# Kernel tuning notes

Hardware: AMD Instinct MI355X
Metric: run time of the kernel (lower is better)

Reference implementation:

```python
import jax, jax.numpy as jnp
import numpy as np

EPS = 1e-5

def _ln(x, g, b):
    m = jnp.mean(x, axis=-1, keepdims=True)
    v = jnp.mean((x - m) ** 2, axis=-1, keepdims=True)
    return (x - m) * jax.lax.rsqrt(v + EPS) * g + b


def setup_inputs() -> dict:
    key = jax.random.key(0)
    B, T, C, H, A = 4, 1024, 1024, 16, 64
    ks = jax.random.split(key, 16)
    s = 0.02
    inp = {
        "x": jax.random.normal(ks[0], (B, T, C), jnp.float32),
        "ln1_g": jnp.ones((C,), jnp.float32), "ln1_b": jnp.zeros((C,), jnp.float32),
        "ln2_g": jnp.ones((C,), jnp.float32), "ln2_b": jnp.zeros((C,), jnp.float32),
        "ln3_g": jnp.ones((C,), jnp.float32), "ln3_b": jnp.zeros((C,), jnp.float32),
        "wq": jax.random.normal(ks[1], (C, C), jnp.float32) * s, "bq": jnp.zeros((C,), jnp.float32),
        "wk": jax.random.normal(ks[2], (C, C), jnp.float32) * s, "bk": jnp.zeros((C,), jnp.float32),
        "wv": jax.random.normal(ks[3], (C, C), jnp.float32) * s, "bv": jnp.zeros((C,), jnp.float32),
        "wo": jax.random.normal(ks[4], (C, C), jnp.float32) * s, "bo": jnp.zeros((C,), jnp.float32),
        "w1": jax.random.normal(ks[5], (C, 4 * C), jnp.float32) * s, "b1": jnp.zeros((4 * C,), jnp.float32),
        "w2": jax.random.normal(ks[6], (4 * C, C), jnp.float32) * s, "b2": jnp.zeros((C,), jnp.float32),
        "wd": jax.random.normal(ks[7], (C, A), jnp.float32) * 1e-4, "bd": jnp.zeros((A,), jnp.float32),
        "wu": jax.random.normal(ks[8], (A, C), jnp.float32) * 1e-4, "bu": jnp.zeros((C,), jnp.float32),
    }
    return inp


def _block(x, ln1_g, ln1_b, ln2_g, ln2_b, ln3_g, ln3_b,
           wq, bq, wk, bk, wv, bv, wo, bo, w1, b1, w2, b2, wd, bd, wu, bu):
    B, T, C = x.shape
    H = 16
    D = C // H
    normed = _ln(x, ln3_g, ln3_b)  # ln3 of original input, used by adapter

    # --- causal self-attention on ln1(x) ---
    h = _ln(x, ln1_g, ln1_b)
    q = (h @ wq + bq).reshape(B, T, H, D)
    k = (h @ wk + bk).reshape(B, T, H, D)
    v = (h @ wv + bv).reshape(B, T, H, D)
    att = jnp.einsum('bqhd,bkhd->bhqk', q, k) * (1.0 / np.sqrt(D))
    causal = jnp.tril(jnp.ones((T, T), bool))
    att = jnp.where(causal, att, -jnp.inf)
    att = jax.nn.softmax(att, axis=-1)
    y = jnp.einsum('bhqk,bkhd->bqhd', att, v).reshape(B, T, C)
    attn_out = y @ wo + bo

    hidden = x + attn_out
    # --- MLP on ln2(hidden) ---
    m = _ln(hidden, ln2_g, ln2_b)
    mlp_out = jax.nn.gelu(m @ w1 + b1, approximate=False) @ w2 + b2
    forward_states = hidden + mlp_out

    # --- adapter on ln3(original x) ---
    a = jax.nn.relu(normed @ wd + bd) @ wu + bu

    # dropout is identity (p=0 / eval)
    return hidden + forward_states + a


def reference(x, ln1_g, ln1_b, ln2_g, ln2_b, ln3_g, ln3_b,
              wq, bq, wk, bk, wv, bv, wo, bo, w1, b1, w2, b2, wd, bd, wu, bu):
    return _block(x, ln1_g, ln1_b, ln2_g, ln2_b, ln3_g, ln3_b,
                  wq, bq, wk, bk, wv, bv, wo, bo, w1, b1, w2, b2, wd, bd, wu, bu)
```

## Files before the change

### kernel.cpp

```cpp
#include <hip/hip_runtime.h>

typedef unsigned short u16;
typedef __bf16 bf16x8 __attribute__((ext_vector_type(8)));
typedef u16    u16x8  __attribute__((ext_vector_type(8)));
typedef float  f32x4  __attribute__((ext_vector_type(4)));

__device__ __forceinline__ u16 f2bf(float f) {
    union { float f; unsigned u; } x{f};
    unsigned r = x.u + 0x7fffu + ((x.u >> 16) & 1u);
    return (u16)(r >> 16);
}

__device__ __forceinline__ f32x4 mfma16(bf16x8 a, bf16x8 b, f32x4 c) {
    return __builtin_amdgcn_mfma_f32_16x16x32_bf16(a, b, c, 0, 0, 0);
}

__global__ void transpose_to_bf16(const float* __restrict__ in, u16* __restrict__ out,
                                  int K, int N) {
    __shared__ float tile[32][33];
    const int k0 = blockIdx.y * 32, n0 = blockIdx.x * 32;
    for (int i = threadIdx.y; i < 32; i += 8)
        tile[i][threadIdx.x] = in[(long)(k0 + i) * N + n0 + threadIdx.x];
    __syncthreads();
    for (int i = threadIdx.y; i < 32; i += 8)
        out[(long)(n0 + i) * K + k0 + threadIdx.x] = f2bf(tile[threadIdx.x][i]);
}

__global__ void concat_bias(const float* __restrict__ bq, const float* __restrict__ bk,
                            const float* __restrict__ bv, float* __restrict__ out) {
    int i = blockIdx.x * 256 + threadIdx.x;
    out[i] = i < 1024 ? bq[i] : (i < 2048 ? bk[i - 1024] : bv[i - 2048]);
}

__global__ void ln_dual_kernel(const float* __restrict__ x,
                               const float* __restrict__ g1, const float* __restrict__ b1,
                               const float* __restrict__ g3, const float* __restrict__ b3,
                               u16* __restrict__ out1, u16* __restrict__ out3) {
    const int row = blockIdx.x;
    const long base = (long)row * 1024;
    const int t = threadIdx.x;
    float4 v = ((const float4*)(x + base))[t];
    float s = v.x + v.y + v.z + v.w;
    float ss = v.x * v.x + v.y * v.y + v.z * v.z + v.w * v.w;
    for (int o = 32; o > 0; o >>= 1) { s += __shfl_down(s, o); ss += __shfl_down(ss, o); }
    __shared__ float red[8];
    if ((t & 63) == 0) { red[t >> 6] = s; red[(t >> 6) + 4] = ss; }
    __syncthreads();
    float sum = red[0] + red[1] + red[2] + red[3];
    float sq  = red[4] + red[5] + red[6] + red[7];
    const float mean = sum * (1.f / 1024.f);
    const float rstd = rsqrtf(sq * (1.f / 1024.f) - mean * mean + 1e-5f);
    float4 G1 = ((const float4*)g1)[t], B1 = ((const float4*)b1)[t];
    float4 G3 = ((const float4*)g3)[t], B3 = ((const float4*)b3)[t];
    float n0 = (v.x - mean) * rstd, n1 = (v.y - mean) * rstd;
    float n2 = (v.z - mean) * rstd, n3 = (v.w - mean) * rstd;
    ushort4 o1, o3;
    o1.x = f2bf(n0 * G1.x + B1.x); o1.y = f2bf(n1 * G1.y + B1.y);
    o1.z = f2bf(n2 * G1.z + B1.z); o1.w = f2bf(n3 * G1.w + B1.w);
    o3.x = f2bf(n0 * G3.x + B3.x); o3.y = f2bf(n1 * G3.y + B3.y);
    o3.z = f2bf(n2 * G3.z + B3.z); o3.w = f2bf(n3 * G3.w + B3.w);
    ((ushort4*)(out1 + base))[t] = o1;
    ((ushort4*)(out3 + base))[t] = o3;
}

__global__ void ln_single_kernel(const float* __restrict__ x,
                                 const float* __restrict__ g, const float* __restrict__ b,
                                 u16* __restrict__ out) {
    const int row = blockIdx.x;
    const long base = (long)row * 1024;
    const int t = threadIdx.x;
    float4 v = ((const float4*)(x + base))[t];
    float s = v.x + v.y + v.z + v.w;
    float ss = v.x * v.x + v.y * v.y + v.z * v.z + v.w * v.w;
    for (int o = 32; o > 0; o >>= 1) { s += __shfl_down(s, o); ss += __shfl_down(ss, o); }
    __shared__ float red[8];
    if ((t & 63) == 0) { red[t >> 6] = s; red[(t >> 6) + 4] = ss; }
    __syncthreads();
    float sum = red[0] + red[1] + red[2] + red[3];
    float sq  = red[4] + red[5] + red[6] + red[7];
    const float mean = sum * (1.f / 1024.f);
    const float rstd = rsqrtf(sq * (1.f / 1024.f) - mean * mean + 1e-5f);
    float4 G = ((const float4*)g)[t], B = ((const float4*)b)[t];
    ushort4 o;
    o.x = f2bf((v.x - mean) * rstd * G.x + B.x);
    o.y = f2bf((v.y - mean) * rstd * G.y + B.y);
    o.z = f2bf((v.z - mean) * rstd * G.z + B.z);
    o.w = f2bf((v.w - mean) * rstd * G.w + B.w);
    ((ushort4*)(out + base))[t] = o;
}

__global__ void transpose_v(const u16* __restrict__ qkv, u16* __restrict__ vT) {
    const int bh = blockIdx.z, b = bh >> 4, hh = bh & 15;
    const int t0 = blockIdx.x * 32, d0 = blockIdx.y * 32;
    __shared__ u16 tile[32][33];
    const u16* src = qkv + (long)(b * 1024) * 3072 + 2048 + hh * 64;
    for (int i = threadIdx.y; i < 32; i += 8)
        tile[i][threadIdx.x] = src[(long)(t0 + i) * 3072 + d0 + threadIdx.x];
    __syncthreads();
    u16* dst = vT + (long)bh * 64 * 1024;
    for (int i = threadIdx.y; i < 32; i += 8)
        dst[(long)(d0 + i) * 1024 + t0 + threadIdx.x] = tile[threadIdx.x][i];
}

template <typename Epi>
__global__ __launch_bounds__(256, 2)
void gemm_kernel(const u16* __restrict__ A, const u16* __restrict__ Bt,
                 int M, int N, int K, Epi epi) {
    __shared__ u16 smA[128 * 32];
    __shared__ u16 smB[128 * 32];
    const int tid = threadIdx.x;
    const int m0 = blockIdx.y * 128;
    const int n0 = blockIdx.x * 128;
    const int wid = tid >> 6, lane = tid & 63;
    const int wm = (wid >> 1) * 64, wn = (wid & 1) * 64;
    const int lr = lane & 15, lh = lane >> 4;

    const int c0 = tid, c1 = tid + 256;
    const int ar0 = c0 >> 2, as0 = (c0 & 3) * 8;
    const int ar1 = c1 >> 2, as1 = (c1 & 3) * 8;
    const long aoff0 = (long)(m0 + ar0) * K + as0;
    const long aoff1 = (long)(m0 + ar1) * K + as1;
    const long boff0 = (long)min(n0 + ar0, N - 1) * K + as0;
    const long boff1 = (long)min(n0 + ar1, N - 1) * K + as1;

    f32x4 acc[4][4] = {};

    uint4 ra0 = *(const uint4*)(A + aoff0);
    uint4 ra1 = *(const uint4*)(A + aoff1);
    uint4 rb0 = *(const uint4*)(Bt + boff0);
    uint4 rb1 = *(const uint4*)(Bt + boff1);

    const int nk = K / 32;
    for (int kt = 0; kt < nk; ++kt) {
        __syncthreads();
        *(uint4*)(smA + c0 * 8) = ra0;
        *(uint4*)(smA + c1 * 8) = ra1;
        *(uint4*)(smB + c0 * 8) = rb0;
        *(uint4*)(smB + c1 * 8) = rb1;
        __syncthreads();
        if (kt + 1 < nk) {
            const int ko = (kt + 1) * 32;
            ra0 = *(const uint4*)(A + aoff0 + ko);
            ra1 = *(const uint4*)(A + aoff1 + ko);
            rb0 = *(const uint4*)(Bt + boff0 + ko);
            rb1 = *(const uint4*)(Bt + boff1 + ko);
        }
        bf16x8 af[4], bfr[4];
#pragma unroll
        for (int i = 0; i < 4; ++i)
            af[i] = *(const bf16x8*)(smA + (wm + i * 16 + lr) * 32 + lh * 8);
#pragma unroll
        for (int j = 0; j < 4; ++j)
            bfr[j] = *(const bf16x8*)(smB + (wn + j * 16 + lr) * 32 + lh * 8);
#pragma unroll
        for (int i = 0; i < 4; ++i)
#pragma unroll
            for (int j = 0; j < 4; ++j)
                acc[i][j] = mfma16(af[i], bfr[j], acc[i][j]);
    }

#pragma unroll
    for (int i = 0; i < 4; ++i)
#pragma unroll
        for (int j = 0; j < 4; ++j) {
            const int col = n0 + wn + j * 16 + lr;
            if (col < N) {
#pragma unroll
                for (int r = 0; r < 4; ++r) {
                    const int row = m0 + wm + i * 16 + lh * 4 + r;
                    epi(row, col, acc[i][j][r]);
                }
            }
        }
}

struct EpiBF16Bias {
    u16* out; const float* bias; int ldo;
    __device__ void operator()(int r, int c, float v) const {
        out[(long)r * ldo + c] = f2bf(v + bias[c]);
    }
};
struct EpiResid {
    float* hidden; const float* bias; const float* x;
    __device__ void operator()(int r, int c, float v) const {
        long i = (long)r * 1024 + c; hidden[i] = v + bias[c] + x[i];
    }
};
struct EpiGelu {
    u16* out; const float* bias;
    __device__ void operator()(int r, int c, float v) const {
        float x = v + bias[c];
        float g = 0.5f * x * (1.f + erff(x * 0.70710678118654752f));
        out[(long)r * 4096 + c] = f2bf(g);
    }
};
struct EpiReluBF16 {
    u16* out; const float* bias;
    __device__ void operator()(int r, int c, float v) const {
        out[(long)r * 64 + c] = f2bf(fmaxf(v + bias[c], 0.f));
    }
};
struct EpiAdapter {
    float* out; const float* bias; const float* hidden;
    __device__ void operator()(int r, int c, float v) const {
        long i = (long)r * 1024 + c; out[i] = 2.f * hidden[i] + v + bias[c];
    }
};
struct EpiAddOut {
    float* out; const float* bias;
    __device__ void operator()(int r, int c, float v) const {
        long i = (long)r * 1024 + c; out[i] += v + bias[c];
    }
};

__global__ __launch_bounds__(256, 2)
void attn_kernel(const u16* __restrict__ qkv, const u16* __restrict__ vT,
                 u16* __restrict__ y) {
    const int bh = blockIdx.x, b = bh >> 4, hh = bh & 15;
    const int q0 = blockIdx.y * 128;
    const int tid = threadIdx.x, wid = tid >> 6, lane = tid & 63;
    const int lr = lane & 15, lh = lane >> 4;
    const int qw = q0 + wid * 32;

    __shared__ u16 smK[64 * 72];
    __shared__ u16 smV[64 * 72];
    __shared__ u16 smP[4 * 32 * 72];
    u16* pw = smP + wid * (32 * 72);

    const u16* qbase = qkv + (long)(b * 1024) * 3072 + hh * 64;
    const u16* kbase = qbase + 1024;
    const u16* vbase = vT + (long)bh * 64 * 1024;

    bf16x8 a_q[2][2];
#pragma unroll
    for (int mt = 0; mt < 2; ++mt)
#pragma unroll
        for (int ks = 0; ks < 2; ++ks) {
            uint4 t = *(const uint4*)(qbase + (long)(qw + mt * 16 + lr) * 3072 + ks * 32 + lh * 8);
            a_q[mt][ks] = __builtin_bit_cast(bf16x8, t);
        }

    bf16x8 ones;
    { u16x8 t = {0x3F80, 0x3F80, 0x3F80, 0x3F80, 0x3F80, 0x3F80, 0x3F80, 0x3F80};
      ones = __builtin_bit_cast(bf16x8, t); }

    f32x4 o_acc[2][4] = {};
    f32x4 l_acc[2] = {};
    f32x4 m_run[2] = {{-1e30f, -1e30f, -1e30f, -1e30f}, {-1e30f, -1e30f, -1e30f, -1e30f}};

    const int ntiles = q0 / 64 + 2;
    const int ck = tid >> 3, cs = (tid & 7) * 8;
    const int ck2 = (tid + 256) >> 3, cs2 = ((tid + 256) & 7) * 8;
    for (int kt = 0; kt < ntiles; ++kt) {
        const int k0 = kt * 64;
        __syncthreads();
        {
            uint4 kv0 = *(const uint4*)(kbase + (long)(k0 + ck) * 3072 + cs);
            uint4 kv1 = *(const uint4*)(kbase + (long)(k0 + ck2) * 3072 + cs2);
            *(uint4*)(smK + ck * 72 + cs) = kv0;
            *(uint4*)(smK + ck2 * 72 + cs2) = kv1;
            uint4 vv0 = *(const uint4*)(vbase + (long)ck * 1024 + k0 + cs);
            uint4 vv1 = *(const uint4*)(vbase + (long)ck2 * 1024 + k0 + cs2);
            *(uint4*)(smV + ck * 72 + cs) = vv0;
            *(uint4*)(smV + ck2 * 72 + cs2) = vv1;
        }
        __syncthreads();
        if (k0 > qw + 31) continue;

        bf16x8 bK[4][2];
#pragma unroll
        for (int nt = 0; nt < 4; ++nt)
#pragma unroll
            for (int ks = 0; ks < 2; ++ks)
                bK[nt][ks] = *(const bf16x8*)(smK + (nt * 16 + lr) * 72 + ks * 32 + lh * 8);

        f32x4 s[2][4];
#pragma unroll
        for (int mt = 0; mt < 2; ++mt)
#pragma unroll
            for (int nt = 0; nt < 4; ++nt) {
                f32x4 z = {0.f, 0.f, 0.f, 0.f};
                z = mfma16(a_q[mt][0], bK[nt][0], z);
                z = mfma16(a_q[mt][1], bK[nt][1], z);
                s[mt][nt] = z;
            }
#pragma unroll
        for (int mt = 0; mt < 2; ++mt) {
            const int qb = qw + mt * 16 + lh * 4;
#pragma unroll
            for (int nt = 0; nt < 4; ++nt) {
                const int kkg = k0 + nt * 16 + lr;
#pragma unroll
                for (int r = 0; r < 4; ++r) {
                    float v = s[mt][nt][r] * 0.125f;
                    if (kkg > qb + r) v = -1e30f;
                    s[mt][nt][r] = v;
                }
            }
        }
#pragma unroll
        for (int mt = 0; mt < 2; ++mt) {
            f32x4 mx = s[mt][0];
#pragma unroll
            for (int nt = 1; nt < 4; ++nt)
#pragma unroll
                for (int r = 0; r < 4; ++r) mx[r] = fmaxf(mx[r], s[mt][nt][r]);
#pragma unroll
            for (int xm = 1; xm < 16; xm <<= 1)
#pragma unroll
                for (int r = 0; r < 4; ++r) mx[r] = fmaxf(mx[r], __shfl_xor(mx[r], xm));
            f32x4 mnew, alpha;
#pragma unroll
            for (int r = 0; r < 4; ++r) {
                mnew[r] = fmaxf(m_run[mt][r], mx[r]);
                alpha[r] = __expf(m_run[mt][r] - mnew[r]);
            }
            m_run[mt] = mnew;
            l_acc[mt] *= alpha;
#pragma unroll
            for (int dt = 0; dt < 4; ++dt) o_acc[mt][dt] *= alpha;
#pragma unroll
            for (int nt = 0; nt < 4; ++nt)
#pragma unroll
                for (int r = 0; r < 4; ++r)
                    s[mt][nt][r] = __expf(s[mt][nt][r] - mnew[r]);
#pragma unroll
            for (int nt = 0; nt < 4; ++nt)
#pragma unroll
                for (int r = 0; r < 4; ++r)
                    pw[(mt * 16 + lh * 4 + r) * 72 + nt * 16 + lr] = f2bf(s[mt][nt][r]);
        }
        bf16x8 vf[4][2];
#pragma unroll
        for (int dt = 0; dt < 4; ++dt)
#pragma unroll
            for (int ks = 0; ks < 2; ++ks)
                vf[dt][ks] = *(const bf16x8*)(smV + (dt * 16 + lr) * 72 + ks * 32 + lh * 8);
#pragma unroll
        for (int mt = 0; mt < 2; ++mt) {
            bf16x8 pf0 = *(const bf16x8*)(pw + (mt * 16 + lr) * 72 + lh * 8);
            bf16x8 pf1 = *(const bf16x8*)(pw + (mt * 16 + lr) * 72 + 32 + lh * 8);
            l_acc[mt] = mfma16(pf0, ones, l_acc[mt]);
            l_acc[mt] = mfma16(pf1, ones, l_acc[mt]);
#pragma unroll
            for (int dt = 0; dt < 4; ++dt) {
                o_acc[mt][dt] = mfma16(pf0, vf[dt][0], o_acc[mt][dt]);
                o_acc[mt][dt] = mfma16(pf1, vf[dt][1], o_acc[mt][dt]);
            }
        }
    }
#pragma unroll
    for (int mt = 0; mt < 2; ++mt) {
        f32x4 linv;
#pragma unroll
        for (int r = 0; r < 4; ++r) linv[r] = 1.f / l_acc[mt][r];
#pragma unroll
        for (int dt = 0; dt < 4; ++dt) {
#pragma unroll
            for (int r = 0; r < 4; ++r) {
                const int tok = b * 1024 + qw + mt * 16 + lh * 4 + r;
                y[(long)tok * 1024 + hh * 64 + dt * 16 + lr] = f2bf(o_acc[mt][dt][r] * linv[r]);
            }
        }
    }
}

extern "C" void kernel_launch(void* const* d_in, const int* in_sizes, int n_in,
                              void* d_out, int out_size, void* d_ws, size_t ws_size,
                              hipStream_t stream) {
    const float* x    = (const float*)d_in[0];
    const float* ln1g = (const float*)d_in[1];
    const float* ln1b = (const float*)d_in[2];
    const float* ln2g = (const float*)d_in[3];
    const float* ln2b = (const float*)d_in[4];
    const float* ln3g = (const float*)d_in[5];
    const float* ln3b = (const float*)d_in[6];
    const float* wq = (const float*)d_in[7];  const float* bq = (const float*)d_in[8];
    const float* wk = (const float*)d_in[9];  const float* bk = (const float*)d_in[10];
    const float* wv = (const float*)d_in[11]; const float* bv = (const float*)d_in[12];
    const float* wo = (const float*)d_in[13]; const float* bo = (const float*)d_in[14];
    const float* w1 = (const float*)d_in[15]; const float* b1 = (const float*)d_in[16];
    const float* w2 = (const float*)d_in[17]; const float* b2 = (const float*)d_in[18];
    const float* wd = (const float*)d_in[19]; const float* bd = (const float*)d_in[20];
    const float* wu = (const float*)d_in[21]; const float* bu = (const float*)d_in[22];
    float* out = (float*)d_out;

    char* base = (char*)d_ws;
    size_t off = 0;
    auto carve = [&](size_t bytes) -> char* {
        char* p = base + off; off += (bytes + 255) & ~(size_t)255; return p;
    };
    u16* qkv_wt = (u16*)carve(3072L * 1024 * 2);
    u16* wo_t   = (u16*)carve(1024L * 1024 * 2);
    u16* w1_t   = (u16*)carve(4096L * 1024 * 2);
    u16* w2_t   = (u16*)carve(1024L * 4096 * 2);
    u16* wd_t   = (u16*)carve(64L * 1024 * 2);
    u16* wu_t   = (u16*)carve(1024L * 64 * 2);
    float* bqkv = (float*)carve(3072L * 4);
    u16* hbuf   = (u16*)carve(4096L * 1024 * 2);
    u16* nrm    = (u16*)carve(4096L * 1024 * 2);
    u16* qkvb   = (u16*)carve(4096L * 3072 * 2);
    u16* vT     = (u16*)carve(64L * 64 * 1024 * 2);
    u16* ybuf   = (u16*)carve(4096L * 1024 * 2);
    float* hid  = (float*)carve(4096L * 1024 * 4);
    u16* mbuf   = (u16*)carve(4096L * 1024 * 2);
    u16* act    = (u16*)carve(4096L * 4096 * 2);
    u16* t1     = (u16*)carve(4096L * 64 * 2);

    const dim3 tb(32, 8);
    transpose_to_bf16<<<dim3(32, 32), tb, 0, stream>>>(wq, qkv_wt, 1024, 1024);
    transpose_to_bf16<<<dim3(32, 32), tb, 0, stream>>>(wk, qkv_wt + 1024L * 1024, 1024, 1024);
    transpose_to_bf16<<<dim3(32, 32), tb, 0, stream>>>(wv, qkv_wt + 2048L * 1024, 1024, 1024);
    transpose_to_bf16<<<dim3(32, 32), tb, 0, stream>>>(wo, wo_t, 1024, 1024);
    transpose_to_bf16<<<dim3(128, 32), tb, 0, stream>>>(w1, w1_t, 1024, 4096);
    transpose_to_bf16<<<dim3(32, 128), tb, 0, stream>>>(w2, w2_t, 4096, 1024);
    transpose_to_bf16<<<dim3(2, 32), tb, 0, stream>>>(wd, wd_t, 1024, 64);
    transpose_to_bf16<<<dim3(32, 2), tb, 0, stream>>>(wu, wu_t, 64, 1024);
    concat_bias<<<12, 256, 0, stream>>>(bq, bk, bv, bqkv);

    ln_dual_kernel<<<4096, 256, 0, stream>>>(x, ln1g, ln1b, ln3g, ln3b, hbuf, nrm);

    gemm_kernel<<<dim3(24, 32), 256, 0, stream>>>(hbuf, qkv_wt, 4096, 3072, 1024,
                                                  EpiBF16Bias{qkvb, bqkv, 3072});
    transpose_v<<<dim3(32, 2, 64), tb, 0, stream>>>(qkvb, vT);
    attn_kernel<<<dim3(64, 8), 256, 0, stream>>>(qkvb, vT, ybuf);
    gemm_kernel<<<dim3(8, 32), 256, 0, stream>>>(ybuf, wo_t, 4096, 1024, 1024,
                                                 EpiResid{hid, bo, x});
    ln_single_kernel<<<4096, 256, 0, stream>>>(hid, ln2g, ln2b, mbuf);
    gemm_kernel<<<dim3(32, 32), 256, 0, stream>>>(mbuf, w1_t, 4096, 4096, 1024,
                                                  EpiGelu{act, b1});
    gemm_kernel<<<dim3(1, 32), 256, 0, stream>>>(nrm, wd_t, 4096, 64, 1024,
                                                 EpiReluBF16{t1, bd});
    gemm_kernel<<<dim3(8, 32), 256, 0, stream>>>(t1, wu_t, 4096, 1024, 64,
                                                 EpiAdapter{out, bu, hid});
    gemm_kernel<<<dim3(8, 32), 256, 0, stream>>>(act, w2_t, 4096, 1024, 4096,
                                                 EpiAddOut{out, b2});
}
```

Measured before the change: 471.0 us.

## Load GEMM tiles directly into LDS with swizzle and widen weight transpose

The GEMM main loop now uses global_load_lds to copy A/B tiles straight from global memory into LDS, replacing the register-staged prefetch. An XOR swizzle on the 16-byte chunks is applied to the LDS layout to avoid bank conflicts on the fragment reads. Launch bounds are raised to 3 blocks per CU. The weight transpose/convert kernel moves to 64x64 tiles with float4 loads and ushort4 stores. The register prefetch that overlapped the next tile's global load with the MFMAs is gone, so load latency is exposed each iteration unless the extra occupancy hides it.

After: 488.4 us. 3.7% more time.

```diff
diff --git a/kernel.cpp b/kernel.cpp
--- a/kernel.cpp
+++ b/kernel.cpp
@@ -15,15 +15,36 @@
     return __builtin_amdgcn_mfma_f32_16x16x32_bf16(a, b, c, 0, 0, 0);
 }
 
+__device__ __forceinline__ void async_ld16(const void* g, void* l) {
+    __builtin_amdgcn_global_load_lds(
+        (const __attribute__((address_space(1))) unsigned int*)g,
+        (__attribute__((address_space(3))) unsigned int*)l, 16, 0, 0);
+}
+
 __global__ void transpose_to_bf16(const float* __restrict__ in, u16* __restrict__ out,
                                   int K, int N) {
-    __shared__ float tile[32][33];
-    const int k0 = blockIdx.y * 32, n0 = blockIdx.x * 32;
-    for (int i = threadIdx.y; i < 32; i += 8)
-        tile[i][threadIdx.x] = in[(long)(k0 + i) * N + n0 + threadIdx.x];
+    __shared__ float tile[64][65];
+    const int k0 = blockIdx.y * 64, n0 = blockIdx.x * 64;
+    const int tid = threadIdx.x;
+    const int rr = tid >> 4, cc = tid & 15;
+#pragma unroll
+    for (int it = 0; it < 4; ++it) {
+        const int r = rr + it * 16;
+        float4 v = *(const float4*)(in + (long)(k0 + r) * N + n0 + cc * 4);
+        tile[r][cc * 4 + 0] = v.x; tile[r][cc * 4 + 1] = v.y;
+        tile[r][cc * 4 + 2] = v.z; tile[r][cc * 4 + 3] = v.w;
+    }
     __syncthreads();
-    for (int i = threadIdx.y; i < 32; i += 8)
-        out[(long)(n0 + i) * K + k0 + threadIdx.x] = f2bf(tile[threadIdx.x][i]);
+#pragma unroll
+    for (int it = 0; it < 4; ++it) {
+        const int n = rr + it * 16;
+        ushort4 o;
+        o.x = f2bf(tile[cc * 4 + 0][n]);
+        o.y = f2bf(tile[cc * 4 + 1][n]);
+        o.z = f2bf(tile[cc * 4 + 2][n]);
+        o.w = f2bf(tile[cc * 4 + 3][n]);
+        *(ushort4*)(out + (long)(n0 + n) * K + k0 + cc * 4) = o;
+    }
 }
 
 __global__ void concat_bias(const float* __restrict__ bq, const float* __restrict__ bk,
@@ -103,7 +124,7 @@
 }
 
 template <typename Epi>
-__global__ __launch_bounds__(256, 2)
+__global__ __launch_bounds__(256, 3)
 void gemm_kernel(const u16* __restrict__ A, const u16* __restrict__ Bt,
                  int M, int N, int K, Epi epi) {
     __shared__ u16 smA[128 * 32];
@@ -115,43 +136,45 @@
     const int wm = (wid >> 1) * 64, wn = (wid & 1) * 64;
     const int lr = lane & 15, lh = lane >> 4;
 
-    const int c0 = tid, c1 = tid + 256;
-    const int ar0 = c0 >> 2, as0 = (c0 & 3) * 8;
-    const int ar1 = c1 >> 2, as1 = (c1 & 3) * 8;
-    const long aoff0 = (long)(m0 + ar0) * K + as0;
-    const long aoff1 = (long)(m0 + ar1) * K + as1;
-    const long boff0 = (long)min(n0 + ar0, N - 1) * K + as0;
-    const long boff1 = (long)min(n0 + ar1, N - 1) * K + as1;
+    const int cr = lane >> 2;
+    const int lq = lane & 3;
+    const int r0 = wid * 32 + cr;
+    const int r1 = wid * 32 + 16 + cr;
+    const int q0 = lq ^ (r0 & 3) ^ ((r0 >> 2) & 3);
+    const int q1 = lq ^ (r1 & 3) ^ ((r1 >> 2) & 3);
+    const int br0 = min(n0 + r0, N - 1);
+    const int br1 = min(n0 + r1, N - 1);
+    const long aoff0 = (long)(m0 + r0) * K + q0 * 8;
+    const long aoff1 = (long)(m0 + r1) * K + q1 * 8;
+    const long boff0 = (long)br0 * K + q0 * 8;
+    const long boff1 = (long)br1 * K + q1 * 8;
+    u16* ldsA0 = smA + (wid * 2    ) * 512;
+    u16* ldsA1 = smA + (wid * 2 + 1) * 512;
+    u16* ldsB0 = smB + (wid * 2    ) * 512;
+    u16* ldsB1 = smB + (wid * 2 + 1) * 512;
+
+    const int rs = (lr & 3) ^ ((lr >> 2) & 3);
+    const int qoff = ((lh ^ rs) & 3) * 8;
 
     f32x4 acc[4][4] = {};
-
-    uint4 ra0 = *(const uint4*)(A + aoff0);
-    uint4 ra1 = *(const uint4*)(A + aoff1);
-    uint4 rb0 = *(const uint4*)(Bt + boff0);
-    uint4 rb1 = *(const uint4*)(Bt + boff1);
 
     const int nk = K / 32;
     for (int kt = 0; kt < nk; ++kt) {
+        const long ko = (long)kt * 32;
         __syncthreads();
-        *(uint4*)(smA + c0 * 8) = ra0;
-        *(uint4*)(smA + c1 * 8) = ra1;
-        *(uint4*)(smB + c0 * 8) = rb0;
-        *(uint4*)(smB + c1 * 8) = rb1;
+        async_ld16(A + aoff0 + ko, ldsA0);
+        async_ld16(A + aoff1 + ko, ldsA1);
+        async_ld16(Bt + boff0 + ko, ldsB0);
+        async_ld16(Bt + boff1 + ko, ldsB1);
         __syncthreads();
-        if (kt + 1 < nk) {
-            const int ko = (kt + 1) * 32;
-            ra0 = *(const uint4*)(A + aoff0 + ko);
-            ra1 = *(const uint4*)(A + aoff1 + ko);
-            rb0 = *(const uint4*)(Bt + boff0 + ko);
-            rb1 = *(const uint4*)(Bt + boff1 + ko);
-        }
+
         bf16x8 af[4], bfr[4];
 #pragma unroll
         for (int i = 0; i < 4; ++i)
-            af[i] = *(const bf16x8*)(smA + (wm + i * 16 + lr) * 32 + lh * 8);
+            af[i] = *(const bf16x8*)(smA + (wm + i * 16 + lr) * 32 + qoff);
 #pragma unroll
         for (int j = 0; j < 4; ++j)
-            bfr[j] = *(const bf16x8*)(smB + (wn + j * 16 + lr) * 32 + lh * 8);
+            bfr[j] = *(const bf16x8*)(smB + (wn + j * 16 + lr) * 32 + qoff);
 #pragma unroll
         for (int i = 0; i < 4; ++i)
 #pragma unroll
@@ -407,22 +430,21 @@
     u16* act    = (u16*)carve(4096L * 4096 * 2);
     u16* t1     = (u16*)carve(4096L * 64 * 2);
 
-    const dim3 tb(32, 8);
-    transpose_to_bf16<<<dim3(32, 32), tb, 0, stream>>>(wq, qkv_wt, 1024, 1024);
-    transpose_to_bf16<<<dim3(32, 32), tb, 0, stream>>>(wk, qkv_wt + 1024L * 1024, 1024, 1024);
-    transpose_to_bf16<<<dim3(32, 32), tb, 0, stream>>>(wv, qkv_wt + 2048L * 1024, 1024, 1024);
-    transpose_to_bf16<<<dim3(32, 32), tb, 0, stream>>>(wo, wo_t, 1024, 1024);
-    transpose_to_bf16<<<dim3(128, 32), tb, 0, stream>>>(w1, w1_t, 1024, 4096);
-    transpose_to_bf16<<<dim3(32, 128), tb, 0, stream>>>(w2, w2_t, 4096, 1024);
-    transpose_to_bf16<<<dim3(2, 32), tb, 0, stream>>>(wd, wd_t, 1024, 64);
-    transpose_to_bf16<<<dim3(32, 2), tb, 0, stream>>>(wu, wu_t, 64, 1024);
+    transpose_to_bf16<<<dim3(16, 16), 256, 0, stream>>>(wq, qkv_wt, 1024, 1024);
+    transpose_to_bf16<<<dim3(16, 16), 256, 0, stream>>>(wk, qkv_wt + 1024L * 1024, 1024, 1024);
+    transpose_to_bf16<<<dim3(16, 16), 256, 0, stream>>>(wv, qkv_wt + 2048L * 1024, 1024, 1024);
+    transpose_to_bf16<<<dim3(16, 16), 256, 0, stream>>>(wo, wo_t, 1024, 1024);
+    transpose_to_bf16<<<dim3(64, 16), 256, 0, stream>>>(w1, w1_t, 1024, 4096);
+    transpose_to_bf16<<<dim3(16, 64), 256, 0, stream>>>(w2, w2_t, 4096, 1024);
+    transpose_to_bf16<<<dim3(1, 16), 256, 0, stream>>>(wd, wd_t, 1024, 64);
+    transpose_to_bf16<<<dim3(16, 1), 256, 0, stream>>>(wu, wu_t, 64, 1024);
     concat_bias<<<12, 256, 0, stream>>>(bq, bk, bv, bqkv);
 
     ln_dual_kernel<<<4096, 256, 0, stream>>>(x, ln1g, ln1b, ln3g, ln3b, hbuf, nrm);
 
     gemm_kernel<<<dim3(24, 32), 256, 0, stream>>>(hbuf, qkv_wt, 4096, 3072, 1024,
                                                   EpiBF16Bias{qkvb, bqkv, 3072});
-    transpose_v<<<dim3(32, 2, 64), tb, 0, stream>>>(qkvb, vT);
+    transpose_v<<<dim3(32, 2, 64), dim3(32, 8), 0, stream>>>(qkvb, vT);
     attn_kernel<<<dim3(64, 8), 256, 0, stream>>>(qkvb, vT, ybuf);
     gemm_kernel<<<dim3(8, 32), 256, 0, stream>>>(ybuf, wo_t, 4096, 1024, 1024,
                                                  EpiResid{hid, bo, x});
```
